# Optimization experiments

Measured on AMD Instinct MI355X. Metric: run time of the kernel, lower is better.

Reference implementation:

```python
import jax, jax.numpy as jnp
import numpy as np

B, T, C = 128, 200, 40      # batch, max visits, codes per visit
N_CODE = 2000               # vocab (token 0 = padding, dropped)
D_AUX = 16
E = 128                     # config.embedding_dim
H_MLP = 256


def setup_inputs() -> dict:
    key = jax.random.key(0)
    ks = jax.random.split(key, 12)
    code = jax.random.randint(ks[0], (B, T, C), 0, N_CODE + 1, dtype=jnp.int32)
    aux_info = jax.random.normal(ks[1], (B, T, D_AUX), dtype=jnp.float32)
    length = jax.random.randint(ks[2], (B,), 1, T + 1, dtype=jnp.int32)
    d_in = N_CODE + D_AUX
    def glorot(k, shape):
        lim = np.sqrt(6.0 / (shape[0] + shape[1]))
        return jax.random.uniform(k, shape, jnp.float32, -lim, lim)
    return {
        "code": code,
        "aux_info": aux_info,
        "length": length,
        "is_training": 0,
        "W_lin": glorot(ks[3], (d_in, E)),
        "b_lin": jnp.zeros((E,), jnp.float32),
        "W_x": glorot(ks[4], (E, 4 * E)),
        "W_h": glorot(ks[5], (E, 4 * E)),
        "b_lstm": jnp.zeros((4 * E,), jnp.float32).at[E:2 * E].set(1.0),  # unit forget bias
        "W0": glorot(ks[6], (E, H_MLP)),
        "b0": jnp.zeros((H_MLP,), jnp.float32),
        "W1": glorot(ks[7], (H_MLP, H_MLP)),
        "b1": jnp.zeros((H_MLP,), jnp.float32),
    }


def _forward(code, aux_info, length, W_lin, b_lin, W_x, W_h, b_lstm, W0, b0, W1, b1):
    Bn, Tn, Cn = code.shape
    # CategoryEncoding binary multi-hot: scatter ones, drop column 0 (padding)
    rows = jnp.repeat(jnp.arange(Bn * Tn), Cn)
    mh = jnp.zeros((Bn * Tn, N_CODE + 1), aux_info.dtype)
    mh = mh.at[rows, code.reshape(-1)].set(1.0)
    mh = mh[:, 1:].reshape(Bn, Tn, N_CODE)
    # Dense + ReLU front-end: [B,T,n+d_aux] @ [d_in,E]
    x = jax.nn.relu(jnp.concatenate([mh, aux_info], axis=-1) @ W_lin + b_lin)
    # LSTM (keras gate order i,f,g,o); inference so dropout inactive
    h0 = jnp.zeros((Bn, W_h.shape[0]), x.dtype)
    def step(carry, xt):
        h, c = carry
        z = xt @ W_x + h @ W_h + b_lstm
        i, f, g, o = jnp.split(z, 4, axis=-1)
        c = jax.nn.sigmoid(f) * c + jax.nn.sigmoid(i) * jnp.tanh(g)
        h = jax.nn.sigmoid(o) * jnp.tanh(c)
        return (h, c), h
    (_, _), hs = jax.lax.scan(step, (h0, h0), x.transpose(1, 0, 2))  # hs: [T,B,E]
    # gather_nd last valid timestep per batch row
    last = hs[length - 1, jnp.arange(Bn)]  # [B,E]
    feat = jax.nn.relu(last @ W0 + b0) @ W1 + b1
    return feat / jnp.sqrt(jnp.sum(feat ** 2, axis=-1, keepdims=True))


def reference(code, aux_info, length, is_training, W_lin, b_lin, W_x, W_h, b_lstm, W0, b0, W1, b1):
    return _forward(code, aux_info, length, W_lin, b_lin, W_x, W_h, b_lstm, W0, b0, W1, b1)
```

## Files before the change

### kernel.cpp

```cpp
#include <hip/hip_runtime.h>
#include <hip/hip_bf16.h>

#define B_    128
#define T_    200
#define C_    40
#define NCODE 2000
#define DAUX  16
#define E_    128
#define H_    256
#define G4    512

__global__ __launch_bounds__(128) void fe_kernel(
    const int* __restrict__ code, const float* __restrict__ aux,
    const float* __restrict__ W_lin, const float* __restrict__ b_lin,
    float* __restrict__ x)
{
    const int cell = blockIdx.x;
    const int e = threadIdx.x;

    __shared__ int codes[C_];
    __shared__ int keep[C_];

    if (e < C_) codes[e] = code[cell * C_ + e];
    __syncthreads();
    if (e < C_) {
        int cj = codes[e];
        int k = (cj != 0);
        for (int i = 0; i < e; ++i)
            if (codes[i] == cj) k = 0;
        keep[e] = k;
    }
    __syncthreads();

    float acc = b_lin[e];
    #pragma unroll 8
    for (int j = 0; j < C_; ++j) {
        int cj = codes[j];
        float w = (float)keep[j];
        int row = (cj > 0) ? (cj - 1) : 0;
        acc = fmaf(w, W_lin[row * E_ + e], acc);
    }
    const float* arow = aux + (size_t)cell * DAUX;
    #pragma unroll
    for (int d = 0; d < DAUX; ++d)
        acc = fmaf(arow[d], W_lin[(NCODE + d) * E_ + e], acc);

    x[(size_t)cell * E_ + e] = fmaxf(acc, 0.f);
}

__global__ __launch_bounds__(256) void gemm_kernel(
    const float* __restrict__ x, const float* __restrict__ Wx,
    const float* __restrict__ bl, float* __restrict__ z)
{
    __shared__ float4 As[64][32];
    __shared__ float4 Bt[64][32];

    const int tid = threadIdx.x;
    const int m0 = blockIdx.x * 64;
    const int n0 = blockIdx.y * 64;

    const float4* x4 = (const float4*)x;
    #pragma unroll
    for (int i = 0; i < 8; ++i) {
        int idx = tid + i * 256;
        int r = idx >> 5, c = idx & 31;
        As[r][c ^ (r & 7)] = x4[(size_t)(m0 + r) * 32 + c];
    }
    #pragma unroll
    for (int i = 0; i < 32; ++i) {
        int idx = tid + i * 256;
        int k = idx >> 6, n = idx & 63;
        ((float*)&Bt[n][(k >> 2) ^ (n & 7)])[k & 3] = Wx[k * G4 + n0 + n];
    }
    __syncthreads();

    const int tn = tid & 15;
    const int tm = tid >> 4;
    float acc[4][4] = {};

    #pragma unroll
    for (int k4 = 0; k4 < 32; ++k4) {
        float4 a[4], bb[4];
        #pragma unroll
        for (int i = 0; i < 4; ++i) {
            int r = 4 * tm + i;
            a[i] = As[r][k4 ^ (r & 7)];
        }
        #pragma unroll
        for (int c = 0; c < 4; ++c)
            bb[c] = Bt[tn + 16 * c][k4 ^ (tn & 7)];
        #pragma unroll
        for (int i = 0; i < 4; ++i)
            #pragma unroll
            for (int c = 0; c < 4; ++c) {
                acc[i][c] = fmaf(a[i].x, bb[c].x, acc[i][c]);
                acc[i][c] = fmaf(a[i].y, bb[c].y, acc[i][c]);
                acc[i][c] = fmaf(a[i].z, bb[c].z, acc[i][c]);
                acc[i][c] = fmaf(a[i].w, bb[c].w, acc[i][c]);
            }
    }

    #pragma unroll
    for (int i = 0; i < 4; ++i) {
        int row = m0 + 4 * tm + i;
        #pragma unroll
        for (int c = 0; c < 4; ++c) {
            int col = n0 + tn + 16 * c;
            z[(size_t)row * G4 + col] = acc[i][c] + bl[col];
        }
    }
}

__global__ __launch_bounds__(512) void lstm_kernel(
    const float* __restrict__ z_pre, const float* __restrict__ Wh,
    const int* __restrict__ length, float* __restrict__ last_h)
{
    const int b = blockIdx.x;
    const int j = threadIdx.x;

    __shared__ float h_lds[E_];
    __shared__ float act[G4];

    float wcol[E_];
    #pragma unroll
    for (int k = 0; k < E_; ++k) wcol[k] = Wh[k * G4 + j];

    if (j < E_) h_lds[j] = 0.f;
    const int len = length[b];
    const float* zp = z_pre + (size_t)b * T_ * G4;
    float c_reg = 0.f;
    float zcur = zp[j];
    __syncthreads();

    for (int t = 0; t < len; ++t) {
        int tnx = (t + 1 < len) ? (t + 1) : t;
        float znext = zp[(size_t)tnx * G4 + j];

        float zv = zcur;
        #pragma unroll
        for (int k = 0; k < E_; ++k)
            zv = fmaf(h_lds[k], wcol[k], zv);

        float a;
        if (j < 2 * E_ || j >= 3 * E_) a = 1.f / (1.f + __expf(-zv));
        else                           a = tanhf(zv);
        act[j] = a;
        __syncthreads();

        if (j < E_) {
            float ai = act[j], af = act[E_ + j], ag = act[2 * E_ + j],
                  ao = act[3 * E_ + j];
            c_reg = af * c_reg + ai * ag;
            float h = ao * tanhf(c_reg);
            h_lds[j] = h;
            if (t == len - 1) last_h[b * E_ + j] = h;
        }
        zcur = znext;
        __syncthreads();
    }
}

__global__ __launch_bounds__(256) void mlp_kernel(
    const float* __restrict__ last_h, const float* __restrict__ W0,
    const float* __restrict__ b0, const float* __restrict__ W1,
    const float* __restrict__ b1, float* __restrict__ out)
{
    const int b = blockIdx.x;
    const int j = threadIdx.x;

    __shared__ float lrow[E_];
    __shared__ float hid[H_];
    __shared__ float red[H_];

    if (j < E_) lrow[j] = last_h[b * E_ + j];
    __syncthreads();

    float a = b0[j];
    #pragma unroll 8
    for (int k = 0; k < E_; ++k)
        a = fmaf(lrow[k], W0[k * H_ + j], a);
    hid[j] = fmaxf(a, 0.f);
    __syncthreads();

    float f = b1[j];
    #pragma unroll 8
    for (int k = 0; k < H_; ++k)
        f = fmaf(hid[k], W1[k * H_ + j], f);

    red[j] = f * f;
    __syncthreads();
    #pragma unroll
    for (int s = 128; s > 0; s >>= 1) {
        if (j < s) red[j] += red[j + s];
        __syncthreads();
    }
    out[(size_t)b * H_ + j] = f / sqrtf(red[0]);
}

extern "C" void kernel_launch(void* const* d_in, const int* in_sizes, int n_in,
                              void* d_out, int out_size, void* d_ws, size_t ws_size,
                              hipStream_t stream)
{
    const int*   code  = (const int*)  d_in[0];
    const float* aux   = (const float*)d_in[1];
    const int*   length= (const int*)  d_in[2];
    const float* W_lin = (const float*)d_in[4];
    const float* b_lin = (const float*)d_in[5];
    const float* W_x   = (const float*)d_in[6];
    const float* W_h   = (const float*)d_in[7];
    const float* b_lstm= (const float*)d_in[8];
    const float* W0    = (const float*)d_in[9];
    const float* b0    = (const float*)d_in[10];
    const float* W1    = (const float*)d_in[11];
    const float* b1    = (const float*)d_in[12];
    float* out = (float*)d_out;

    char* ws = (char*)d_ws;
    float* x      = (float*)ws;
    float* z_pre  = (float*)(ws + (size_t)B_ * T_ * E_ * 4);
    float* last_h = (float*)(ws + (size_t)B_ * T_ * E_ * 4
                                + (size_t)B_ * T_ * G4 * 4);

    fe_kernel<<<B_ * T_, 128, 0, stream>>>(code, aux, W_lin, b_lin, x);
    gemm_kernel<<<dim3((B_ * T_) / 64, G4 / 64), 256, 0, stream>>>(x, W_x, b_lstm, z_pre);
    lstm_kernel<<<B_, 512, 0, stream>>>(z_pre, W_h, length, last_h);
    mlp_kernel<<<B_, H_, 0, stream>>>(last_h, W0, b0, W1, b1, out);
}
```

Baseline: 356.9 us.

## Skip padded timesteps and restructure LSTM recurrence with per-thread gate groups

The front-end and input-projection GEMM now skip work for timesteps beyond each sequence's length, since the LSTM never reads them. The LSTM kernel is reorganized so each group of 4 threads owns one hidden unit and all four of its gates, splitting K across the threads and reducing with shuffles. This removes the activation round-trip through shared memory and one of the two barriers per step, and double-buffers h. Fast sigmoid and tanh approximations replace tanhf, which introduces small precision differences.

Result: faster. 339.4 us (-4.9%).

```diff
diff --git a/kernel.cpp b/kernel.cpp
--- a/kernel.cpp
+++ b/kernel.cpp
@@ -10,13 +10,29 @@
 #define H_    256
 #define G4    512
 
+__device__ __forceinline__ float sigmoid_fast(float x) {
+    return __fdividef(1.f, 1.f + __expf(-x));
+}
+__device__ __forceinline__ float tanh_fast(float x) {
+    x = fminf(15.f, fmaxf(-15.f, x));
+    float e = __expf(2.f * x);
+    return __fdividef(e - 1.f, e + 1.f);
+}
+
 __global__ __launch_bounds__(128) void fe_kernel(
     const int* __restrict__ code, const float* __restrict__ aux,
     const float* __restrict__ W_lin, const float* __restrict__ b_lin,
-    float* __restrict__ x)
+    const int* __restrict__ length, float* __restrict__ x)
 {
     const int cell = blockIdx.x;
     const int e = threadIdx.x;
+    const int b = cell / T_;
+    const int t = cell - b * T_;
+
+    if (t >= length[b]) {
+        x[(size_t)cell * E_ + e] = 0.f;
+        return;
+    }
 
     __shared__ int codes[C_];
     __shared__ int keep[C_];
@@ -50,14 +66,23 @@
 
 __global__ __launch_bounds__(256) void gemm_kernel(
     const float* __restrict__ x, const float* __restrict__ Wx,
-    const float* __restrict__ bl, float* __restrict__ z)
-{
+    const float* __restrict__ bl, const int* __restrict__ length,
+    float* __restrict__ z)
+{
+    const int m0 = blockIdx.x * 64;
+    const int n0 = blockIdx.y * 64;
+
+    {
+        int b_first = m0 / T_;
+        int b_last  = (m0 + 63) / T_;
+        if (b_first == b_last && (m0 - b_first * T_) >= length[b_first])
+            return;
+    }
+
     __shared__ float4 As[64][32];
     __shared__ float4 Bt[64][32];
 
     const int tid = threadIdx.x;
-    const int m0 = blockIdx.x * 64;
-    const int n0 = blockIdx.y * 64;
 
     const float4* x4 = (const float4*)x;
     #pragma unroll
@@ -115,47 +140,70 @@
     const float* __restrict__ z_pre, const float* __restrict__ Wh,
     const int* __restrict__ length, float* __restrict__ last_h)
 {
-    const int b = blockIdx.x;
-    const int j = threadIdx.x;
-
-    __shared__ float h_lds[E_];
-    __shared__ float act[G4];
-
-    float wcol[E_];
-    #pragma unroll
-    for (int k = 0; k < E_; ++k) wcol[k] = Wh[k * G4 + j];
-
-    if (j < E_) h_lds[j] = 0.f;
+    const int b  = blockIdx.x;
+    const int tid = threadIdx.x;
+    const int j  = tid >> 2;
+    const int ks = tid & 3;
+
+    __shared__ float h_lds[2][E_];
+
+    float w0[32], w1[32], w2[32], w3[32];
+    #pragma unroll
+    for (int kk = 0; kk < 32; ++kk) {
+        const float* row = Wh + (size_t)(32 * ks + kk) * G4 + j;
+        w0[kk] = row[0];
+        w1[kk] = row[E_];
+        w2[kk] = row[2 * E_];
+        w3[kk] = row[3 * E_];
+    }
+
     const int len = length[b];
     const float* zp = z_pre + (size_t)b * T_ * G4;
+
+    if (tid < E_) h_lds[0][tid] = 0.f;
     float c_reg = 0.f;
-    float zcur = zp[j];
-    __syncthreads();
-
-    for (int t = 0; t < len; ++t) {
-        int tnx = (t + 1 < len) ? (t + 1) : t;
-        float znext = zp[(size_t)tnx * G4 + j];
-
-        float zv = zcur;
-        #pragma unroll
-        for (int k = 0; k < E_; ++k)
-            zv = fmaf(h_lds[k], wcol[k], zv);
-
-        float a;
-        if (j < 2 * E_ || j >= 3 * E_) a = 1.f / (1.f + __expf(-zv));
-        else                           a = tanhf(zv);
-        act[j] = a;
-        __syncthreads();
-
-        if (j < E_) {
-            float ai = act[j], af = act[E_ + j], ag = act[2 * E_ + j],
-                  ao = act[3 * E_ + j];
-            c_reg = af * c_reg + ai * ag;
-            float h = ao * tanhf(c_reg);
-            h_lds[j] = h;
-            if (t == len - 1) last_h[b * E_ + j] = h;
-        }
-        zcur = znext;
+    float z0 = zp[j], z1 = zp[E_ + j], z2 = zp[2 * E_ + j], z3 = zp[3 * E_ + j];
+    __syncthreads();
+
+    for (int s = 0; s < len; ++s) {
+        const int cur = s & 1, nxt = cur ^ 1;
+
+        const int tn = (s + 1 < len) ? s + 1 : s;
+        const float* zn = zp + (size_t)tn * G4;
+        float p0 = zn[j], p1 = zn[E_ + j], p2 = zn[2 * E_ + j], p3 = zn[3 * E_ + j];
+
+        float hreg[32];
+        #pragma unroll
+        for (int q = 0; q < 8; ++q)
+            *(float4*)&hreg[4 * q] = *(const float4*)&h_lds[cur][32 * ks + 4 * q];
+
+        float a0 = 0.f, a1 = 0.f, a2 = 0.f, a3 = 0.f;
+        #pragma unroll
+        for (int kk = 0; kk < 32; ++kk) {
+            float h = hreg[kk];
+            a0 = fmaf(h, w0[kk], a0);
+            a1 = fmaf(h, w1[kk], a1);
+            a2 = fmaf(h, w2[kk], a2);
+            a3 = fmaf(h, w3[kk], a3);
+        }
+        a0 += __shfl_xor(a0, 1); a0 += __shfl_xor(a0, 2);
+        a1 += __shfl_xor(a1, 1); a1 += __shfl_xor(a1, 2);
+        a2 += __shfl_xor(a2, 1); a2 += __shfl_xor(a2, 2);
+        a3 += __shfl_xor(a3, 1); a3 += __shfl_xor(a3, 2);
+        a0 += z0; a1 += z1; a2 += z2; a3 += z3;
+
+        float ig = sigmoid_fast(a0);
+        float fg = sigmoid_fast(a1);
+        float gg = tanh_fast(a2);
+        float og = sigmoid_fast(a3);
+        c_reg = fg * c_reg + ig * gg;
+        float h = og * tanh_fast(c_reg);
+
+        if (ks == 0) {
+            h_lds[nxt][j] = h;
+            if (s == len - 1) last_h[b * E_ + j] = h;
+        }
+        z0 = p0; z1 = p1; z2 = p2; z3 = p3;
         __syncthreads();
     }
 }
@@ -221,8 +269,8 @@
     float* last_h = (float*)(ws + (size_t)B_ * T_ * E_ * 4
                                 + (size_t)B_ * T_ * G4 * 4);
 
-    fe_kernel<<<B_ * T_, 128, 0, stream>>>(code, aux, W_lin, b_lin, x);
-    gemm_kernel<<<dim3((B_ * T_) / 64, G4 / 64), 256, 0, stream>>>(x, W_x, b_lstm, z_pre);
+    fe_kernel<<<B_ * T_, 128, 0, stream>>>(code, aux, W_lin, b_lin, length, x);
+    gemm_kernel<<<dim3((B_ * T_) / 64, G4 / 64), 256, 0, stream>>>(x, W_x, b_lstm, length, z_pre);
     lstm_kernel<<<B_, 512, 0, stream>>>(z_pre, W_h, length, last_h);
     mlp_kernel<<<B_, H_, 0, stream>>>(last_h, W0, b0, W1, b1, out);
 }
```
